# Kernel optimization log

Hardware: AMD Instinct MI355X
Metric: run time of the kernel (lower is better)

The kernel has to match this reference:

```python
import jax, jax.numpy as jnp
import numpy as np

N_HEAD = 8
NORM_GROUPS = 32
EPS = 1e-6


def setup_inputs() -> dict:
    key = jax.random.key(0)
    ks = jax.random.split(key, 9)
    B, C, H, W, D = 1, 256, 16, 16, 16
    COND = 512
    x = jax.random.normal(ks[0], (B, C, H, W, D), dtype=jnp.float32)
    cond = jax.random.normal(ks[1], (B, COND), dtype=jnp.float32)
    # AdaGN linear scale/shift (torch Linear: weight [C, cond_dim], bias [C])
    w_scale = jax.random.normal(ks[2], (C, COND), dtype=jnp.float32) * 0.02
    b_scale = jax.random.normal(ks[3], (C,), dtype=jnp.float32) * 0.02
    w_shift = jax.random.normal(ks[4], (C, COND), dtype=jnp.float32) * 0.02
    b_shift = jax.random.normal(ks[5], (C,), dtype=jnp.float32) * 0.02
    # 1x1x1 conv3d weights collapse to matrices: qkv [3C, C] (no bias), out [C, C] + bias
    w_qkv = jax.random.normal(ks[6], (3 * C, C), dtype=jnp.float32) * (1.0 / np.sqrt(C))
    w_out = jax.random.normal(ks[7], (C, C), dtype=jnp.float32) * (1.0 / np.sqrt(C))
    b_out = jax.random.normal(ks[8], (C,), dtype=jnp.float32) * 0.02
    return {"x": x, "cond": cond, "w_scale": w_scale, "b_scale": b_scale,
            "w_shift": w_shift, "b_shift": b_shift, "w_qkv": w_qkv,
            "w_out": w_out, "b_out": b_out}


def _ada_gn(x, cond, w_scale, b_scale, w_shift, b_shift):
    B, C, H, W, D = x.shape
    G = NORM_GROUPS
    xg = x.reshape(B, G, C // G, H, W, D)
    mean = jnp.mean(xg, axis=(2, 3, 4, 5), keepdims=True)
    var = jnp.var(xg, axis=(2, 3, 4, 5), keepdims=True)
    x_norm = ((xg - mean) * jax.lax.rsqrt(var + EPS)).reshape(B, C, H, W, D)
    scale = (cond @ w_scale.T + b_scale)[:, :, None, None, None]  # [B,C,1,1,1]
    shift = (cond @ w_shift.T + b_shift)[:, :, None, None, None]
    return x_norm * (1.0 + scale) + shift


def reference(x, cond, w_scale, b_scale, w_shift, b_shift, w_qkv, w_out, b_out):
    B, C, H, W, D = x.shape
    nh = N_HEAD
    hd = C // nh
    N = H * W * D  # flattened spatial tokens
    norm = _ada_gn(x, cond, w_scale, b_scale, w_shift, b_shift)
    # 1x1x1 conv == channel matmul
    qkv = jnp.einsum('oc,bchwd->bohwd', w_qkv, norm)        # [B,3C,H,W,D]
    qkv = qkv.reshape(B, nh, 3 * hd, N)
    q, k, v = jnp.split(qkv, 3, axis=2)                      # each [B,nh,hd,N]
    attn = jnp.einsum('bnci,bncj->bnij', q, k) / jnp.sqrt(jnp.float32(C))
    attn = jax.nn.softmax(attn, axis=-1)                     # [B,nh,N,N]
    out = jnp.einsum('bnij,bncj->bnci', attn, v)             # [B,nh,hd,N]
    out = out.reshape(B, C, H, W, D)
    out = jnp.einsum('oc,bchwd->bohwd', w_out, out) + b_out[None, :, None, None, None]
    return out + x
```

## Files before the change

### kernel.cpp

```cpp
#include <hip/hip_runtime.h>
#include <math.h>

#define CCH 256
#define NN  4096
#define NHEAD 8
#define CONDD 512

typedef __attribute__((ext_vector_type(8))) short short8;
typedef __attribute__((ext_vector_type(4))) float f32x4;
typedef __attribute__((ext_vector_type(16))) float f32x16;

static __device__ __forceinline__ short f2bf(float f) {
    union { float f; uint32_t u; } v; v.f = f;
    uint32_t r = v.u + 0x7fffu + ((v.u >> 16) & 1u);
    return (short)(r >> 16);
}

static __device__ __forceinline__ uint32_t cvt_pk_bf16(float a, float b) {
    uint32_t r;
    asm("v_cvt_pk_bf16_f32 %0, %1, %2" : "=v"(r) : "v"(a), "v"(b));
    return r;
}

__global__ __launch_bounds__(256) void front_fused(const float* __restrict__ x,
                                                   const float* __restrict__ cond,
                                                   const float* __restrict__ w_scale,
                                                   const float* __restrict__ b_scale,
                                                   const float* __restrict__ w_shift,
                                                   const float* __restrict__ b_shift,
                                                   const float* __restrict__ wq,
                                                   const float* __restrict__ wo,
                                                   float* __restrict__ partial,
                                                   float* __restrict__ scale,
                                                   float* __restrict__ shift,
                                                   short* __restrict__ wqb,
                                                   short* __restrict__ wob) {
    __shared__ float rs[4], rss[4];
    int bb = blockIdx.x;
    int t = threadIdx.x;
    if (bb < 256) {
        const float4* p = (const float4*)(x + bb * 4096);
        float s = 0.f, ss = 0.f;
        for (int k = t; k < 1024; k += 256) {
            float4 v = p[k];
            s += v.x + v.y + v.z + v.w;
            ss += v.x * v.x + v.y * v.y + v.z * v.z + v.w * v.w;
        }
        #pragma unroll
        for (int off = 32; off; off >>= 1) { s += __shfl_xor(s, off); ss += __shfl_xor(ss, off); }
        int wid = t >> 6;
        if ((t & 63) == 0) { rs[wid] = s; rss[wid] = ss; }
        __syncthreads();
        if (t == 0) {
            partial[2 * bb] = rs[0] + rs[1] + rs[2] + rs[3];
            partial[2 * bb + 1] = rss[0] + rss[1] + rss[2] + rss[3];
        }
    } else if (bb < 1280) {
        int idx = (bb - 256) * 256 + t;
        if (idx < 196608) wqb[idx] = f2bf(wq[idx]);
        else              wob[idx - 196608] = f2bf(wo[idx - 196608]);
    } else {
        int o = (bb - 1280) * 4 + (t >> 6);
        int lane = t & 63;
        float ds = 0.f, dh = 0.f;
        for (int k = lane; k < CONDD; k += 64) {
            float cv = cond[k];
            ds += cv * w_scale[o * CONDD + k];
            dh += cv * w_shift[o * CONDD + k];
        }
        #pragma unroll
        for (int off = 32; off; off >>= 1) { ds += __shfl_xor(ds, off); dh += __shfl_xor(dh, off); }
        if (lane == 0) { scale[o] = ds + b_scale[o]; shift[o] = dh + b_shift[o]; }
    }
}

__global__ __launch_bounds__(256) void normalize_t(const float* __restrict__ x,
                                                   const float* __restrict__ partial,
                                                   const float* __restrict__ scale,
                                                   const float* __restrict__ shift,
                                                   short* __restrict__ norm_t) {
    __shared__ float gm[8], gr[8];
    __shared__ float Aa[64], Bb[64];
    __shared__ short tile[32 * 66];
    int i0 = blockIdx.x * 32;
    int c0 = blockIdx.y * 64;
    int g0 = c0 >> 3;
    int t = threadIdx.x;
    if (t < 8) {
        float s = 0.f, ss = 0.f;
        #pragma unroll
        for (int ch = 0; ch < 8; ++ch) {
            s += partial[((g0 + t) * 8 + ch) * 2];
            ss += partial[((g0 + t) * 8 + ch) * 2 + 1];
        }
        float mean = s * (1.0f / 32768.0f);
        float var = ss * (1.0f / 32768.0f) - mean * mean;
        gm[t] = mean;
        gr[t] = rsqrtf(var + 1e-6f);
    }
    __syncthreads();
    if (t < 64) {
        int c = c0 + t;
        float a = gr[t >> 3] * (1.0f + scale[c]);
        Aa[t] = a;
        Bb[t] = shift[c] - gm[t >> 3] * a;
    }
    __syncthreads();
    #pragma unroll
    for (int e0 = 0; e0 < 8; ++e0) {
        int e = e0 * 256 + t;
        int cl = e >> 5, il = e & 31;
        float v = x[(c0 + cl) * NN + i0 + il];
        tile[il * 66 + cl] = f2bf(v * Aa[cl] + Bb[cl]);
    }
    __syncthreads();
    #pragma unroll
    for (int e0 = 0; e0 < 4; ++e0) {
        int e = e0 * 256 + t;
        int il = e >> 5, cd = e & 31;
        uint32_t d = *(const uint32_t*)&tile[il * 66 + 2 * cd];
        *(uint32_t*)&norm_t[(i0 + il) * 256 + c0 + 2 * cd] = d;
    }
}

__global__ __launch_bounds__(256) void qkv_gemm(const short* __restrict__ wqb,
                                                const short* __restrict__ norm_t,
                                                short* __restrict__ qtb, short* __restrict__ ktb,
                                                short* __restrict__ vcb) {
    int t = threadIdx.x;
    int w = t >> 6, lane = t & 63, li = lane & 15, lg = lane >> 4;
    int o0 = blockIdx.x * 32;
    int i0 = blockIdx.y * 64 + w * 16;
    f32x4 acc[2] = {{0,0,0,0},{0,0,0,0}};
    const short* bbase = norm_t + (i0 + li) * 256 + 8 * lg;
    const short* abase = wqb + (o0 + li) * 256 + 8 * lg;
    #pragma unroll
    for (int ks = 0; ks < 8; ++ks) {
        short8 bfrag = *(const short8*)(bbase + ks * 32);
        #pragma unroll
        for (int f = 0; f < 2; ++f) {
            short8 afrag = *(const short8*)(abase + f * 16 * 256 + ks * 32);
            acc[f] = __builtin_amdgcn_mfma_f32_16x16x32_bf16(afrag, bfrag, acc[f], 0, 0, 0);
        }
    }
    int i = i0 + li;
    #pragma unroll
    for (int f = 0; f < 2; ++f) {
        #pragma unroll
        for (int r = 0; r < 4; ++r) {
            int o = o0 + 16 * f + 4 * lg + r;
            float v = acc[f][r];
            int h = o / 96;
            int rr = o - h * 96;
            int cc = rr & 31;
            int kind = rr >> 5;
            if (kind == 0)      qtb[(h * NN + i) * 32 + cc] = f2bf(v * (0.0625f * 1.44269504f));
            else if (kind == 1) ktb[(h * NN + i) * 32 + cc] = f2bf(v);
            else                vcb[(h * 32 + cc) * NN + i] = f2bf(v);
        }
    }
}

__global__ __launch_bounds__(256, 4) void attention_mfma(const short* __restrict__ qtb,
                                                         const short* __restrict__ ktb,
                                                         const short* __restrict__ vcb,
                                                         float* __restrict__ pacc,
                                                         float* __restrict__ plsum) {
    __shared__ __align__(16) short kbuf[2][2][2048];
    __shared__ __align__(16) short vbuf[2][2][2048];

    int bid = blockIdx.x;
    int h = bid & 7;
    int qb = (bid >> 3) & 31;
    int kh = bid >> 8;
    int t = threadIdx.x;
    int w = t >> 6, lane = t & 63, l31 = lane & 31, hi = lane >> 5;

    int qbase = qb * 128 + w * 32;
    const short* qrow = qtb + (h * NN + qbase + l31) * 32;
    short8 qf0 = *(const short8*)(qrow + 8 * hi);
    short8 qf1 = *(const short8*)(qrow + 16 + 8 * hi);

    int kr_ = t >> 2, ks_ = t & 3, kg_ = ks_ ^ (kr_ & 3);
    int vr_ = t >> 3, vs_ = t & 7, vg_ = vs_ ^ (vr_ & 7);
    const char* kgbase = (const char*)(ktb + (h * NN + kh * 1024) * 32) + kr_ * 64 + kg_ * 16;
    const char* vgbase = (const char*)(vcb + (h * 32 + vr_) * NN + kh * 1024) + vg_ * 16;
    int wave_off = w * 1024;

    f32x16 acc = {0,0,0,0,0,0,0,0,0,0,0,0,0,0,0,0};
    const f32x16 zero16 = {0,0,0,0,0,0,0,0,0,0,0,0,0,0,0,0};
    float lsum = 0.f;

    __builtin_amdgcn_global_load_lds((const uint32_t*)(kgbase),        (uint32_t*)((char*)&kbuf[0][0][0] + wave_off), 16, 0, 0);
    __builtin_amdgcn_global_load_lds((const uint32_t*)(kgbase + 4096), (uint32_t*)((char*)&kbuf[0][1][0] + wave_off), 16, 0, 0);
    __builtin_amdgcn_global_load_lds((const uint32_t*)(vgbase),        (uint32_t*)((char*)&vbuf[0][0][0] + wave_off), 16, 0, 0);
    __builtin_amdgcn_global_load_lds((const uint32_t*)(vgbase + 128),  (uint32_t*)((char*)&vbuf[0][1][0] + wave_off), 16, 0, 0);
    __syncthreads();

    #pragma unroll 1
    for (int st = 0; st < 8; ++st) {
        int cur = st & 1;
        if (st < 7) {
            const char* kn = kgbase + (st + 1) * 8192;
            const char* vn = vgbase + (st + 1) * 256;
            __builtin_amdgcn_global_load_lds((const uint32_t*)(kn),        (uint32_t*)((char*)&kbuf[cur ^ 1][0][0] + wave_off), 16, 0, 0);
            __builtin_amdgcn_global_load_lds((const uint32_t*)(kn + 4096), (uint32_t*)((char*)&kbuf[cur ^ 1][1][0] + wave_off), 16, 0, 0);
            __builtin_amdgcn_global_load_lds((const uint32_t*)(vn),        (uint32_t*)((char*)&vbuf[cur ^ 1][0][0] + wave_off), 16, 0, 0);
            __builtin_amdgcn_global_load_lds((const uint32_t*)(vn + 128),  (uint32_t*)((char*)&vbuf[cur ^ 1][1][0] + wave_off), 16, 0, 0);
        }

        #pragma unroll
        for (int chunk = 0; chunk < 2; ++chunk) {
            #pragma unroll
            for (int half = 0; half < 2; ++half) {
                int jl = half * 32;
                int R = jl + l31;
                const short* kr = &kbuf[cur][chunk][R * 32];
                int rx = R & 3;
                short8 kf0 = *(const short8*)(kr + ((hi ^ rx) << 3));
                short8 kf1 = *(const short8*)(kr + (((2 + hi) ^ rx) << 3));
                const short* vr = &vbuf[cur][chunk][l31 * 64];
                int cx = l31 & 7;
                int s0 = (jl >> 3) + hi;
                short8 vf0 = *(const short8*)(vr + ((s0 ^ cx) << 3));
                short8 vf1 = *(const short8*)(vr + (((s0 + 2) ^ cx) << 3));

                __builtin_amdgcn_s_setprio(1);
                f32x16 s = __builtin_amdgcn_mfma_f32_32x32x16_bf16(kf0, qf0, zero16, 0, 0, 0);
                s = __builtin_amdgcn_mfma_f32_32x32x16_bf16(kf1, qf1, s, 0, 0, 0);
                __builtin_amdgcn_s_setprio(0);

                float p[16];
                #pragma unroll
                for (int r = 0; r < 16; ++r) p[r] = __builtin_amdgcn_exp2f(s[r]);

                float u0 = 0.f, u1 = 0.f;
                #pragma unroll
                for (int r = 0; r < 4; ++r) { u0 += p[r] + p[4 + r]; u1 += p[8 + r] + p[12 + r]; }
                lsum += u0 + u1;

                auto A1 = __builtin_amdgcn_permlane32_swap(cvt_pk_bf16(p[0], p[1]),   cvt_pk_bf16(p[4], p[5]),   false, false);
                auto A2 = __builtin_amdgcn_permlane32_swap(cvt_pk_bf16(p[2], p[3]),   cvt_pk_bf16(p[6], p[7]),   false, false);
                auto A3 = __builtin_amdgcn_permlane32_swap(cvt_pk_bf16(p[8], p[9]),   cvt_pk_bf16(p[12], p[13]), false, false);
                auto A4 = __builtin_amdgcn_permlane32_swap(cvt_pk_bf16(p[10], p[11]), cvt_pk_bf16(p[14], p[15]), false, false);

                union PF { uint32_t u[4]; short8 s8; };
                PF f1, f2;
                f1.u[0] = A1[0]; f1.u[1] = A2[0]; f1.u[2] = A1[1]; f1.u[3] = A2[1];
                f2.u[0] = A3[0]; f2.u[1] = A4[0]; f2.u[2] = A3[1]; f2.u[3] = A4[1];

                __builtin_amdgcn_s_setprio(1);
                acc = __builtin_amdgcn_mfma_f32_32x32x16_bf16(vf0, f1.s8, acc, 0, 0, 0);
                acc = __builtin_amdgcn_mfma_f32_32x32x16_bf16(vf1, f2.s8, acc, 0, 0, 0);
                __builtin_amdgcn_s_setprio(0);
            }
        }
        __syncthreads();
    }

    lsum += __shfl_xor(lsum, 32);

    int qg = qbase + l31;
    float* pb = pacc + ((kh * 8 + h) * 32) * NN + qg;
    #pragma unroll
    for (int r = 0; r < 16; ++r) {
        int c = (r & 3) + 8 * (r >> 2) + 4 * hi;
        pb[c * NN] = acc[r];
    }
    if (hi == 0) plsum[(kh * 8 + h) * NN + qg] = lsum;
}

__global__ __launch_bounds__(256) void attn_merge(const float* __restrict__ pacc,
                                                  const float* __restrict__ plsum,
                                                  short* __restrict__ attnT) {
    __shared__ float tile[64][33];
    __shared__ float invl[64];
    int it = blockIdx.x;
    int h = blockIdx.y;
    int t = threadIdx.x;
    int i0 = it * 64;
    int c = t >> 3, ic = (t & 7) * 8;
    const float* p0 = pacc + (h * 32 + c) * NN + i0 + ic;
    #pragma unroll
    for (int k = 0; k < 8; ++k) {
        float s = 0.f;
        #pragma unroll
        for (int q4 = 0; q4 < 4; ++q4) s += p0[q4 * 8 * 32 * NN + k];
        tile[ic + k][c] = s;
    }
    if (t < 64) {
        float ls = 0.f;
        #pragma unroll
        for (int q4 = 0; q4 < 4; ++q4) ls += plsum[(q4 * 8 + h) * NN + i0 + t];
        invl[t] = 1.0f / ls;
    }
    __syncthreads();
    int i = t >> 2, cs = (t & 3) * 8;
    float iv = invl[i];
    const float* tr = &tile[i][cs];
    uint4 o;
    o.x = cvt_pk_bf16(tr[0] * iv, tr[1] * iv);
    o.y = cvt_pk_bf16(tr[2] * iv, tr[3] * iv);
    o.z = cvt_pk_bf16(tr[4] * iv, tr[5] * iv);
    o.w = cvt_pk_bf16(tr[6] * iv, tr[7] * iv);
    *(uint4*)&attnT[(i0 + i) * 256 + h * 32 + cs] = o;
}

__global__ __launch_bounds__(256) void proj_gemm(const short* __restrict__ wob,
                                                 const short* __restrict__ attnT,
                                                 const float* __restrict__ b_out,
                                                 const float* __restrict__ x,
                                                 float* __restrict__ out) {
    int t = threadIdx.x;
    int w = t >> 6, lane = t & 63, li = lane & 15, lg = lane >> 4;
    int o0 = blockIdx.x * 32;
    int i0 = blockIdx.y * 64 + w * 16;
    f32x4 acc[2] = {{0,0,0,0},{0,0,0,0}};
    const short* bbase = attnT + (i0 + li) * 256 + 8 * lg;
    const short* abase = wob + (o0 + li) * 256 + 8 * lg;
    #pragma unroll
    for (int ks = 0; ks < 8; ++ks) {
        short8 bfrag = *(const short8*)(bbase + ks * 32);
        #pragma unroll
        for (int f = 0; f < 2; ++f) {
            short8 afrag = *(const short8*)(abase + f * 16 * 256 + ks * 32);
            acc[f] = __builtin_amdgcn_mfma_f32_16x16x32_bf16(afrag, bfrag, acc[f], 0, 0, 0);
        }
    }
    int i = i0 + li;
    #pragma unroll
    for (int f = 0; f < 2; ++f) {
        #pragma unroll
        for (int r = 0; r < 4; ++r) {
            int o = o0 + 16 * f + 4 * lg + r;
            out[o * NN + i] = acc[f][r] + b_out[o] + x[o * NN + i];
        }
    }
}

extern "C" void kernel_launch(void* const* d_in, const int* in_sizes, int n_in,
                              void* d_out, int out_size, void* d_ws, size_t ws_size,
                              hipStream_t stream) {
    const float* x       = (const float*)d_in[0];
    const float* cond    = (const float*)d_in[1];
    const float* w_scale = (const float*)d_in[2];
    const float* b_scale = (const float*)d_in[3];
    const float* w_shift = (const float*)d_in[4];
    const float* b_shift = (const float*)d_in[5];
    const float* w_qkv   = (const float*)d_in[6];
    const float* w_out   = (const float*)d_in[7];
    const float* b_out   = (const float*)d_in[8];
    float* out = (float*)d_out;

    float* ws = (float*)d_ws;
    float* scale   = ws;
    float* shift   = ws + 256;
    float* partial = ws + 512;
    short* norm_t = (short*)(ws + 1024);
    short* qtb = norm_t + 1048576;
    short* ktb = qtb + 1048576;
    short* vcb = ktb + 1048576;
    short* attnT = vcb + 1048576;
    short* wqb = attnT + 1048576;
    short* wob = wqb + 768 * 256;
    float* pacc  = (float*)(wob + 65536);
    float* plsum = pacc + 4 * 8 * 32 * NN;

    front_fused<<<1344, 256, 0, stream>>>(x, cond, w_scale, b_scale, w_shift, b_shift,
                                          w_qkv, w_out, partial, scale, shift, wqb, wob);
    normalize_t<<<dim3(128, 4), 256, 0, stream>>>(x, partial, scale, shift, norm_t);
    qkv_gemm<<<dim3(24, 64), 256, 0, stream>>>(wqb, norm_t, qtb, ktb, vcb);
    attention_mfma<<<1024, 256, 0, stream>>>(qtb, ktb, vcb, pacc, plsum);
    attn_merge<<<dim3(64, 8), 256, 0, stream>>>(pacc, plsum, attnT);
    proj_gemm<<<dim3(8, 64), 256, 0, stream>>>(wob, attnT, b_out, x, out);
}
```

Measured before the change: 72.68 us.

## Use 512-thread attention blocks with triple-buffered LDS and role-split loaders

The attention kernel now runs 512-thread blocks covering 256 queries each, halving the grid so every K/V tile loaded into LDS serves twice as many query rows. Loads move from a double-buffered to a triple-buffered ring of 48KB, with waves 0-3 loading K and waves 4-7 loading V, and a fully unrolled schedule using explicit vmcnt waits and s_barrier instead of __syncthreads. The aim is to cut global K/V traffic and hide load latency behind more compute. The costs are larger LDS use per block and the requirement that 4 blocks of 512 threads fit per CU, which may cut occupancy, plus more fragile hand-written wait counts.

```diff
diff --git a/kernel.cpp b/kernel.cpp
--- a/kernel.cpp
+++ b/kernel.cpp
@@ -161,102 +161,132 @@
     }
 }
 
-__global__ __launch_bounds__(256, 4) void attention_mfma(const short* __restrict__ qtb,
+__global__ __launch_bounds__(512, 4) void attention_mfma(const short* __restrict__ qtb,
                                                          const short* __restrict__ ktb,
                                                          const short* __restrict__ vcb,
                                                          float* __restrict__ pacc,
                                                          float* __restrict__ plsum) {
-    __shared__ __align__(16) short kbuf[2][2][2048];
-    __shared__ __align__(16) short vbuf[2][2][2048];
+    __shared__ __align__(16) char lds[49152];
 
     int bid = blockIdx.x;
     int h = bid & 7;
-    int qb = (bid >> 3) & 31;
-    int kh = bid >> 8;
+    int qb = (bid >> 3) & 15;
+    int kh = bid >> 7;
     int t = threadIdx.x;
     int w = t >> 6, lane = t & 63, l31 = lane & 31, hi = lane >> 5;
 
-    int qbase = qb * 128 + w * 32;
+    int qbase = qb * 256 + w * 32;
     const short* qrow = qtb + (h * NN + qbase + l31) * 32;
     short8 qf0 = *(const short8*)(qrow + 8 * hi);
     short8 qf1 = *(const short8*)(qrow + 16 + 8 * hi);
-
-    int kr_ = t >> 2, ks_ = t & 3, kg_ = ks_ ^ (kr_ & 3);
-    int vr_ = t >> 3, vs_ = t & 7, vg_ = vs_ ^ (vr_ & 7);
-    const char* kgbase = (const char*)(ktb + (h * NN + kh * 1024) * 32) + kr_ * 64 + kg_ * 16;
-    const char* vgbase = (const char*)(vcb + (h * 32 + vr_) * NN + kh * 1024) + vg_ * 16;
-    int wave_off = w * 1024;
+    asm volatile("s_waitcnt vmcnt(0)" ::: "memory");
+
+    const char* src0;
+    const char* src1;
+    int ldsoff0, ldsoff1, step;
+    if (w < 4) {
+        int row_l = lane >> 2, g_lds = lane & 3;
+        int g_glob = g_lds ^ (row_l & 3);
+        const char* kbase = (const char*)ktb + (size_t)(h * NN + kh * 1024) * 64;
+        int s0 = 2 * w, s1 = 2 * w + 1;
+        src0 = kbase + ((s0 >> 2) * 64 + (s0 & 3) * 16 + row_l) * 64 + g_glob * 16;
+        src1 = kbase + ((s1 >> 2) * 64 + (s1 & 3) * 16 + row_l) * 64 + g_glob * 16;
+        ldsoff0 = s0 * 1024;
+        ldsoff1 = s1 * 1024;
+        step = 8192;
+    } else {
+        int row_l = lane >> 3, vs_lds = lane & 7;
+        int vg = vs_lds ^ row_l;
+        const char* vbase = (const char*)vcb + (size_t)(h * 32) * (NN * 2) + kh * 2048;
+        int s0 = 2 * (w - 4), s1 = 2 * (w - 4) + 1;
+        src0 = vbase + (size_t)((s0 & 3) * 8 + row_l) * (NN * 2) + (s0 >> 2) * 128 + vg * 16;
+        src1 = vbase + (size_t)((s1 & 3) * 8 + row_l) * (NN * 2) + (s1 >> 2) * 128 + vg * 16;
+        ldsoff0 = 8192 + s0 * 1024;
+        ldsoff1 = 8192 + s1 * 1024;
+        step = 256;
+    }
 
     f32x16 acc = {0,0,0,0,0,0,0,0,0,0,0,0,0,0,0,0};
     const f32x16 zero16 = {0,0,0,0,0,0,0,0,0,0,0,0,0,0,0,0};
     float lsum = 0.f;
 
-    __builtin_amdgcn_global_load_lds((const uint32_t*)(kgbase),        (uint32_t*)((char*)&kbuf[0][0][0] + wave_off), 16, 0, 0);
-    __builtin_amdgcn_global_load_lds((const uint32_t*)(kgbase + 4096), (uint32_t*)((char*)&kbuf[0][1][0] + wave_off), 16, 0, 0);
-    __builtin_amdgcn_global_load_lds((const uint32_t*)(vgbase),        (uint32_t*)((char*)&vbuf[0][0][0] + wave_off), 16, 0, 0);
-    __builtin_amdgcn_global_load_lds((const uint32_t*)(vgbase + 128),  (uint32_t*)((char*)&vbuf[0][1][0] + wave_off), 16, 0, 0);
-    __syncthreads();
-
-    #pragma unroll 1
-    for (int st = 0; st < 8; ++st) {
-        int cur = st & 1;
-        if (st < 7) {
-            const char* kn = kgbase + (st + 1) * 8192;
-            const char* vn = vgbase + (st + 1) * 256;
-            __builtin_amdgcn_global_load_lds((const uint32_t*)(kn),        (uint32_t*)((char*)&kbuf[cur ^ 1][0][0] + wave_off), 16, 0, 0);
-            __builtin_amdgcn_global_load_lds((const uint32_t*)(kn + 4096), (uint32_t*)((char*)&kbuf[cur ^ 1][1][0] + wave_off), 16, 0, 0);
-            __builtin_amdgcn_global_load_lds((const uint32_t*)(vn),        (uint32_t*)((char*)&vbuf[cur ^ 1][0][0] + wave_off), 16, 0, 0);
-            __builtin_amdgcn_global_load_lds((const uint32_t*)(vn + 128),  (uint32_t*)((char*)&vbuf[cur ^ 1][1][0] + wave_off), 16, 0, 0);
-        }
-
-        #pragma unroll
-        for (int chunk = 0; chunk < 2; ++chunk) {
-            #pragma unroll
-            for (int half = 0; half < 2; ++half) {
-                int jl = half * 32;
-                int R = jl + l31;
-                const short* kr = &kbuf[cur][chunk][R * 32];
-                int rx = R & 3;
-                short8 kf0 = *(const short8*)(kr + ((hi ^ rx) << 3));
-                short8 kf1 = *(const short8*)(kr + (((2 + hi) ^ rx) << 3));
-                const short* vr = &vbuf[cur][chunk][l31 * 64];
-                int cx = l31 & 7;
-                int s0 = (jl >> 3) + hi;
-                short8 vf0 = *(const short8*)(vr + ((s0 ^ cx) << 3));
-                short8 vf1 = *(const short8*)(vr + (((s0 + 2) ^ cx) << 3));
-
-                __builtin_amdgcn_s_setprio(1);
-                f32x16 s = __builtin_amdgcn_mfma_f32_32x32x16_bf16(kf0, qf0, zero16, 0, 0, 0);
-                s = __builtin_amdgcn_mfma_f32_32x32x16_bf16(kf1, qf1, s, 0, 0, 0);
-                __builtin_amdgcn_s_setprio(0);
-
-                float p[16];
-                #pragma unroll
-                for (int r = 0; r < 16; ++r) p[r] = __builtin_amdgcn_exp2f(s[r]);
-
-                float u0 = 0.f, u1 = 0.f;
-                #pragma unroll
-                for (int r = 0; r < 4; ++r) { u0 += p[r] + p[4 + r]; u1 += p[8 + r] + p[12 + r]; }
-                lsum += u0 + u1;
-
-                auto A1 = __builtin_amdgcn_permlane32_swap(cvt_pk_bf16(p[0], p[1]),   cvt_pk_bf16(p[4], p[5]),   false, false);
-                auto A2 = __builtin_amdgcn_permlane32_swap(cvt_pk_bf16(p[2], p[3]),   cvt_pk_bf16(p[6], p[7]),   false, false);
-                auto A3 = __builtin_amdgcn_permlane32_swap(cvt_pk_bf16(p[8], p[9]),   cvt_pk_bf16(p[12], p[13]), false, false);
-                auto A4 = __builtin_amdgcn_permlane32_swap(cvt_pk_bf16(p[10], p[11]), cvt_pk_bf16(p[14], p[15]), false, false);
-
-                union PF { uint32_t u[4]; short8 s8; };
-                PF f1, f2;
-                f1.u[0] = A1[0]; f1.u[1] = A2[0]; f1.u[2] = A1[1]; f1.u[3] = A2[1];
-                f2.u[0] = A3[0]; f2.u[1] = A4[0]; f2.u[2] = A3[1]; f2.u[3] = A4[1];
-
-                __builtin_amdgcn_s_setprio(1);
-                acc = __builtin_amdgcn_mfma_f32_32x32x16_bf16(vf0, f1.s8, acc, 0, 0, 0);
-                acc = __builtin_amdgcn_mfma_f32_32x32x16_bf16(vf1, f2.s8, acc, 0, 0, 0);
-                __builtin_amdgcn_s_setprio(0);
-            }
-        }
-        __syncthreads();
-    }
+    #define ISSUE(st, b) do { \
+        __builtin_amdgcn_global_load_lds((const uint32_t*)(src0 + (st) * step), \
+            (uint32_t*)(lds + (b) * 16384 + ldsoff0), 16, 0, 0); \
+        __builtin_amdgcn_global_load_lds((const uint32_t*)(src1 + (st) * step), \
+            (uint32_t*)(lds + (b) * 16384 + ldsoff1), 16, 0, 0); \
+    } while (0)
+
+    #define COMPUTE(b) do { \
+        const char* bb_ = lds + (b) * 16384; \
+        _Pragma("unroll") \
+        for (int chunk = 0; chunk < 2; ++chunk) { \
+            _Pragma("unroll") \
+            for (int half = 0; half < 2; ++half) { \
+                int jl = half * 32; \
+                int R = jl + l31; \
+                int rx = R & 3; \
+                const char* kr = bb_ + chunk * 4096 + R * 64; \
+                short8 kf0 = *(const short8*)(kr + (((hi) ^ rx) << 4)); \
+                short8 kf1 = *(const short8*)(kr + (((2 + hi) ^ rx) << 4)); \
+                const char* vr = bb_ + 8192 + chunk * 4096 + l31 * 128; \
+                int cx = l31 & 7; \
+                int sv = (jl >> 3) + hi; \
+                short8 vf0 = *(const short8*)(vr + ((sv ^ cx) << 4)); \
+                short8 vf1 = *(const short8*)(vr + (((sv + 2) ^ cx) << 4)); \
+                __builtin_amdgcn_s_setprio(1); \
+                f32x16 s = __builtin_amdgcn_mfma_f32_32x32x16_bf16(kf0, qf0, zero16, 0, 0, 0); \
+                s = __builtin_amdgcn_mfma_f32_32x32x16_bf16(kf1, qf1, s, 0, 0, 0); \
+                __builtin_amdgcn_s_setprio(0); \
+                float p[16]; \
+                _Pragma("unroll") \
+                for (int r = 0; r < 16; ++r) p[r] = __builtin_amdgcn_exp2f(s[r]); \
+                float u0 = 0.f, u1 = 0.f; \
+                _Pragma("unroll") \
+                for (int r = 0; r < 4; ++r) { u0 += p[r] + p[4 + r]; u1 += p[8 + r] + p[12 + r]; } \
+                lsum += u0 + u1; \
+                auto A1 = __builtin_amdgcn_permlane32_swap(cvt_pk_bf16(p[0], p[1]),   cvt_pk_bf16(p[4], p[5]),   false, false); \
+                auto A2 = __builtin_amdgcn_permlane32_swap(cvt_pk_bf16(p[2], p[3]),   cvt_pk_bf16(p[6], p[7]),   false, false); \
+                auto A3 = __builtin_amdgcn_permlane32_swap(cvt_pk_bf16(p[8], p[9]),   cvt_pk_bf16(p[12], p[13]), false, false); \
+                auto A4 = __builtin_amdgcn_permlane32_swap(cvt_pk_bf16(p[10], p[11]), cvt_pk_bf16(p[14], p[15]), false, false); \
+                union PF { uint32_t u[4]; short8 s8; }; \
+                PF f1, f2; \
+                f1.u[0] = A1[0]; f1.u[1] = A2[0]; f1.u[2] = A1[1]; f1.u[3] = A2[1]; \
+                f2.u[0] = A3[0]; f2.u[1] = A4[0]; f2.u[2] = A3[1]; f2.u[3] = A4[1]; \
+                __builtin_amdgcn_s_setprio(1); \
+                acc = __builtin_amdgcn_mfma_f32_32x32x16_bf16(vf0, f1.s8, acc, 0, 0, 0); \
+                acc = __builtin_amdgcn_mfma_f32_32x32x16_bf16(vf1, f2.s8, acc, 0, 0, 0); \
+                __builtin_amdgcn_s_setprio(0); \
+            } \
+        } \
+    } while (0)
+
+    ISSUE(0, 0);
+    ISSUE(1, 1);
+    ISSUE(2, 2);
+    asm volatile("s_waitcnt vmcnt(4)" ::: "memory");
+    __builtin_amdgcn_s_barrier();
+
+    #pragma unroll
+    for (int st = 0; st < 5; ++st) {
+        COMPUTE(st % 3);
+        __builtin_amdgcn_s_barrier();
+        ISSUE(st + 3, st % 3);
+        asm volatile("s_waitcnt vmcnt(4)" ::: "memory");
+        __builtin_amdgcn_s_barrier();
+    }
+    COMPUTE(2);
+    __builtin_amdgcn_s_barrier();
+    asm volatile("s_waitcnt vmcnt(2)" ::: "memory");
+    __builtin_amdgcn_s_barrier();
+    COMPUTE(0);
+    __builtin_amdgcn_s_barrier();
+    asm volatile("s_waitcnt vmcnt(0)" ::: "memory");
+    __builtin_amdgcn_s_barrier();
+    COMPUTE(1);
+
+    #undef ISSUE
+    #undef COMPUTE
 
     lsum += __shfl_xor(lsum, 32);
 
@@ -370,7 +400,7 @@
                                           w_qkv, w_out, partial, scale, shift, wqb, wob);
     normalize_t<<<dim3(128, 4), 256, 0, stream>>>(x, partial, scale, shift, norm_t);
     qkv_gemm<<<dim3(24, 64), 256, 0, stream>>>(wqb, norm_t, qtb, ktb, vcb);
-    attention_mfma<<<1024, 256, 0, stream>>>(qtb, ktb, vcb, pacc, plsum);
+    attention_mfma<<<512, 512, 0, stream>>>(qtb, ktb, vcb, pacc, plsum);
     attn_merge<<<dim3(64, 8), 256, 0, stream>>>(pacc, plsum, attnT);
     proj_gemm<<<dim3(8, 64), 256, 0, stream>>>(wob, attnT, b_out, x, out);
 }
```

Result: faster. 70.54 us (-3.0%).
